# Performance work log

Hardware: AMD Instinct MI355X
Metric: run time of the kernel (lower is better)

## Reference

```python
import jax, jax.numpy as jnp
import numpy as np

B, S, D, H = 2, 2048, 2048, 16
HD = D // H
FF = 4 * D
EPS = 1e-5
SCALE = 1.0 / np.sqrt(D)  # source uses 1/sqrt(d_out), not 1/sqrt(head_dim)


def _gelu_tanh(x):
    c = np.sqrt(2.0 / np.pi).astype(np.float32)
    return 0.5 * x * (1.0 + jnp.tanh(c * (x + 0.044715 * x * x * x)))


def _layernorm(x, scale, shift):
    mean = jnp.mean(x, axis=-1, keepdims=True)
    var = jnp.mean(jnp.square(x - mean), axis=-1, keepdims=True)  # correction=0
    return (x - mean) * jax.lax.rsqrt(var + EPS) * scale + shift


def setup_inputs() -> dict:
    key = jax.random.key(0)
    ks = jax.random.split(key, 10)
    init = lambda k, shape, fan_in: (jax.random.normal(k, shape, jnp.float32) / np.sqrt(fan_in))
    return {
        "x": jax.random.normal(ks[0], (B, S, D), jnp.float32),
        "wq": init(ks[1], (D, D), D),
        "wk": init(ks[2], (D, D), D),
        "wv": init(ks[3], (D, D), D),
        "wo": init(ks[4], (D, D), D),
        "bo": jnp.zeros((D,), jnp.float32),
        "g1": jnp.ones((D,), jnp.float32),
        "s1": jnp.zeros((D,), jnp.float32),
        "g2": jnp.ones((D,), jnp.float32),
        "s2": jnp.zeros((D,), jnp.float32),
        "w1": init(ks[5], (D, FF), D),
        "b1": jnp.zeros((FF,), jnp.float32),
        "w2": init(ks[6], (FF, D), FF),
        "b2": jnp.zeros((D,), jnp.float32),
    }


def _block(x, wq, wk, wv, wo, bo, g1, s1, g2, s2, w1, b1, w2, b2):
    # pre-LN attention
    h = _layernorm(x, g1, s1)
    q = (h @ wq).reshape(B, S, H, HD).transpose(0, 2, 1, 3)  # [B,H,S,HD]
    k = (h @ wk).reshape(B, S, H, HD).transpose(0, 2, 1, 3)
    v = (h @ wv).reshape(B, S, H, HD).transpose(0, 2, 1, 3)
    scores = jnp.einsum('bhqd,bhkd->bhqk', q, k) * SCALE
    causal = jnp.tril(jnp.ones((S, S), dtype=bool))  # mask strictly-upper
    scores = jnp.where(causal, scores, -jnp.inf)
    attn = jax.nn.softmax(scores, axis=-1)
    ctx = jnp.einsum('bhqk,bhkd->bhqd', attn, v)
    ctx = ctx.transpose(0, 2, 1, 3).reshape(B, S, D)
    x = x + ctx @ wo + bo
    # pre-LN FFN
    h = _layernorm(x, g2, s2)
    h = _gelu_tanh(h @ w1 + b1) @ w2 + b2
    return x + h


def reference(x, wq, wk, wv, wo, bo, g1, s1, g2, s2, w1, b1, w2, b2):
    return _block(x, wq, wk, wv, wo, bo, g1, s1, g2, s2, w1, b1, w2, b2)
```

## Files before the change

kernel.cpp:

```cpp
#include <hip/hip_runtime.h>
#include <hip/hip_bf16.h>
#include <cstdint>

constexpr float SCALE_QK = 0.02209708691207961f;

using short8 = __attribute__((ext_vector_type(8))) short;
using f32x4  = __attribute__((ext_vector_type(4))) float;
using ushort4v = __attribute__((ext_vector_type(4))) ushort;

#define MFMA16(a,b,c) __builtin_amdgcn_mfma_f32_16x16x32_bf16((a),(b),(c),0,0,0)

__device__ __forceinline__ ushort f2bf(float f){
  uint32_t u = __builtin_bit_cast(uint32_t, f);
  u += 0x7fffu + ((u >> 16) & 1u);
  return (ushort)(u >> 16);
}

__device__ __forceinline__ void gload_lds16(const void* g, void* l){
  __builtin_amdgcn_global_load_lds(
      (const __attribute__((address_space(1))) void*)g,
      (__attribute__((address_space(3))) void*)l, 16, 0, 0);
}

__global__ __launch_bounds__(256) void ln_kernel(
    const float* __restrict__ x, const float* __restrict__ g,
    const float* __restrict__ sh, ushort* __restrict__ out){
  const int row = blockIdx.x, t = threadIdx.x;
  const float* xr = x + (size_t)row*2048 + t*8;
  float v[8];
  *(float4*)&v[0] = *(const float4*)(xr);
  *(float4*)&v[4] = *(const float4*)(xr + 4);
  float s = 0.f, sq = 0.f;
#pragma unroll
  for (int i = 0; i < 8; ++i){ s += v[i]; sq += v[i]*v[i]; }
#pragma unroll
  for (int d = 1; d < 64; d <<= 1){ s += __shfl_xor(s, d, 64); sq += __shfl_xor(sq, d, 64); }
  __shared__ float red[8];
  const int w = t >> 6, lane = t & 63;
  if (lane == 0){ red[w] = s; red[4 + w] = sq; }
  __syncthreads();
  s  = red[0] + red[1] + red[2] + red[3];
  sq = red[4] + red[5] + red[6] + red[7];
  const float mean = s * (1.f/2048.f);
  const float inv  = rsqrtf(sq * (1.f/2048.f) - mean*mean + 1e-5f);
  union { ushort u[8]; uint4 v4; } o;
#pragma unroll
  for (int i = 0; i < 8; ++i){
    int j = t*8 + i;
    o.u[i] = f2bf((v[i] - mean) * inv * g[j] + sh[j]);
  }
  *(uint4*)(out + (size_t)row*2048 + t*8) = o.v4;
}

__global__ __launch_bounds__(256) void wconv_t(
    const float* __restrict__ in, ushort* __restrict__ out, int K, int N){
  __shared__ ushort tile[32][34];
  const int tx = threadIdx.x & 31, ty = threadIdx.x >> 5;
  const int n0 = blockIdx.x * 32, k0 = blockIdx.y * 32;
#pragma unroll
  for (int r = 0; r < 4; ++r){
    int kk = ty + r*8;
    tile[kk][tx] = f2bf(in[(size_t)(k0 + kk)*N + n0 + tx]);
  }
  __syncthreads();
#pragma unroll
  for (int r = 0; r < 4; ++r){
    int nn = ty + r*8;
    out[(size_t)(n0 + nn)*K + k0 + tx] = tile[tx][nn];
  }
}

template<int EPI>
__global__ __launch_bounds__(256) void gemm_bt(
    const ushort* __restrict__ A, const ushort* __restrict__ Bt,
    int N, int K, void* __restrict__ outp,
    const float* __restrict__ resid, const float* __restrict__ bias){
  __shared__ ushort lds[2][128*64];
  const int tid = threadIdx.x, lane = tid & 63, wid = tid >> 6;
  const int wr = wid >> 1, wc = wid & 1;
  const int l15 = lane & 15, l4 = lane >> 4;

  const int bid = blockIdx.x;
  const int xcd = bid & 7, j = bid >> 3;
  const int mb = xcd*4 + (j & 3);
  const int nb = j >> 2;
  const int m0 = mb * 128, n0 = nb * 128;

  f32x4 acc[4][4];
#pragma unroll
  for (int mi = 0; mi < 4; ++mi)
#pragma unroll
    for (int ni = 0; ni < 4; ++ni) acc[mi][ni] = (f32x4){0.f,0.f,0.f,0.f};

  const ushort* Abase = A  + (size_t)m0*K;
  const ushort* Bbase = Bt + (size_t)n0*K;

  const int NTk = K >> 6;
  for (int kt = 0; kt < NTk; ++kt){
    if (kt) __syncthreads();
#pragma unroll
    for (int i = 0; i < 4; ++i){
      const int chunk = (i*4 + wid)*64 + lane;
      const int row = chunk >> 3;
      const int c8  = (chunk & 7) ^ (row & 7);
      const size_t goff = (size_t)row*K + (size_t)kt*64 + c8*8;
      gload_lds16(Abase + goff, (ushort*)&lds[0][0] + (size_t)(i*4 + wid)*512);
      gload_lds16(Bbase + goff, (ushort*)&lds[1][0] + (size_t)(i*4 + wid)*512);
    }
    __syncthreads();

#pragma unroll
    for (int kk = 0; kk < 2; ++kk){
      short8 af[4], bf[4];
      const int kb = kk*4 + l4;
#pragma unroll
      for (int i = 0; i < 4; ++i){
        const int rA = wr*64 + i*16 + l15;
        af[i] = *(const short8*)&lds[0][rA*64 + ((kb ^ (rA & 7))*8)];
        const int rB = wc*64 + i*16 + l15;
        bf[i] = *(const short8*)&lds[1][rB*64 + ((kb ^ (rB & 7))*8)];
      }
#pragma unroll
      for (int mi = 0; mi < 4; ++mi)
#pragma unroll
        for (int ni = 0; ni < 4; ++ni)
          acc[mi][ni] = MFMA16(af[mi], bf[ni], acc[mi][ni]);
    }
  }

#pragma unroll
  for (int mi = 0; mi < 4; ++mi){
#pragma unroll
    for (int ni = 0; ni < 4; ++ni){
      const int rloc = wr*64 + mi*16 + l4*4;
      const int col  = n0 + wc*64 + ni*16 + l15;
      if constexpr (EPI == 0){
        const int which = col >> 11, rest = col & 2047;
        const int h = rest >> 7, d = rest & 127;
        const int mrow = m0 + rloc;
        const int b = mrow >> 11, s = mrow & 2047;
        if (which == 2){
          ushort4v o;
#pragma unroll
          for (int j2 = 0; j2 < 4; ++j2) o[j2] = f2bf(acc[mi][ni][j2]);
          *(ushort4v*)&((ushort*)outp)[(size_t)2*8388608 +
              (size_t)(b*16 + h)*262144 + (size_t)d*2048 + s] = o;
        } else {
#pragma unroll
          for (int j2 = 0; j2 < 4; ++j2)
            ((ushort*)outp)[(size_t)which*8388608 +
                (((size_t)(b*16 + h)*2048 + (s + j2)) << 7) + d] = f2bf(acc[mi][ni][j2]);
        }
      } else {
#pragma unroll
        for (int j2 = 0; j2 < 4; ++j2){
          const int m = m0 + rloc + j2;
          float v = acc[mi][ni][j2];
          if constexpr (EPI == 1){
            ((float*)outp)[(size_t)m*N + col] = resid[(size_t)m*N + col] + bias[col] + v;
          } else {
            const float xx = v + bias[col];
            const float z  = 0.7978845608f*(xx + 0.044715f*xx*xx*xx);
            const float t  = __expf(-2.f*fabsf(z));
            const float th = (1.f - t)/(1.f + t);
            const float gl = 0.5f*xx*(1.f + copysignf(th, xx));
            ((ushort*)outp)[(size_t)m*N + col] = f2bf(gl);
          }
        }
      }
    }
  }
}

__global__ __launch_bounds__(256, 2) void attn_kernel(
    const ushort* __restrict__ q, const ushort* __restrict__ k,
    const ushort* __restrict__ vt, ushort* __restrict__ ctx){
  __shared__ ushort k_lds[2][64*128];
  __shared__ ushort v_lds[2][128*64];
  __shared__ ushort p_lds[4][32*64];
  const int tid = threadIdx.x, lane = tid & 63, w = tid >> 6;
  const int l15 = lane & 15, l4 = lane >> 4;
  const int id = blockIdx.x;
  const int bh = id & 31;
  const int r  = id >> 5;
  const int qt = (r < 8) ? (15 - r) : (r - 8);
  const int bb = bh >> 4, hh = bh & 15;
  const ushort* kbase = k  + (size_t)bh * 262144;
  const ushort* vbase = vt + (size_t)bh * 262144;

  short8 qf[2][4];
#pragma unroll
  for (int mi = 0; mi < 2; ++mi){
    const int s = qt*128 + w*32 + mi*16 + l15;
    const ushort* qr = q + ((size_t)bh*2048 + s)*128 + l4*8;
#pragma unroll
    for (int kk = 0; kk < 4; ++kk) qf[mi][kk] = *(const short8*)(qr + kk*32);
  }

  f32x4 cacc[2][8];
#pragma unroll
  for (int mi = 0; mi < 2; ++mi)
#pragma unroll
    for (int dt = 0; dt < 8; ++dt) cacc[mi][dt] = (f32x4){0.f,0.f,0.f,0.f};
  float mrun[2][4], lrun[2][4];
#pragma unroll
  for (int mi = 0; mi < 2; ++mi)
#pragma unroll
    for (int j = 0; j < 4; ++j){ mrun[mi][j] = -1e30f; lrun[mi][j] = 0.f; }

  auto stage = [&](int buf, int t){
    const ushort* ksrc = kbase + (size_t)t*8192;
#pragma unroll
    for (int i = 0; i < 4; ++i){
      const int base = i*256 + w*64;
      const int chunk = base + lane;
      const int kr = chunk >> 4;
      const int c8 = (chunk & 15) ^ (kr & 7);
      gload_lds16(ksrc + (size_t)kr*128 + c8*8, &k_lds[buf][(size_t)base*8]);
    }
#pragma unroll
    for (int i = 0; i < 4; ++i){
      const int base = i*256 + w*64;
      const int chunk = base + lane;
      const int vr = chunk >> 3;
      const int c8 = (chunk & 7) ^ (vr & 7);
      gload_lds16(vbase + (size_t)vr*2048 + t*64 + c8*8, &v_lds[buf][(size_t)base*8]);
    }
  };

  const int nt = 2*qt + 2;
  stage(0, 0);
  __syncthreads();
  int cur = 0;
  for (int t = 0; t < nt; ++t){
    if (t + 1 < nt) stage(cur ^ 1, t + 1);

    f32x4 sa[2][4];
#pragma unroll
    for (int mi = 0; mi < 2; ++mi)
#pragma unroll
      for (int ct = 0; ct < 4; ++ct) sa[mi][ct] = (f32x4){0.f,0.f,0.f,0.f};
    __builtin_amdgcn_s_setprio(1);
#pragma unroll
    for (int kk = 0; kk < 4; ++kk){
#pragma unroll
      for (int ct = 0; ct < 4; ++ct){
        const int kr = ct*16 + l15;
        short8 kf = *(const short8*)&k_lds[cur][kr*128 + (((kk*4 + l4) ^ (kr & 7))*8)];
        sa[0][ct] = MFMA16(qf[0][kk], kf, sa[0][ct]);
        sa[1][ct] = MFMA16(qf[1][kk], kf, sa[1][ct]);
      }
    }
    __builtin_amdgcn_s_setprio(0);

    const bool diag = (t >= 2*qt);
#pragma unroll
    for (int mi = 0; mi < 2; ++mi){
#pragma unroll
      for (int j = 0; j < 4; ++j){
        const int qa = qt*128 + w*32 + mi*16 + l4*4 + j;
        float mnew = mrun[mi][j];
#pragma unroll
        for (int ct = 0; ct < 4; ++ct){
          float sc = sa[mi][ct][j] * SCALE_QK;
          if (diag){
            const int ka = t*64 + ct*16 + l15;
            sc = (ka > qa) ? -1e30f : sc;
          }
          sa[mi][ct][j] = sc;
          mnew = fmaxf(mnew, sc);
        }
#pragma unroll
        for (int d = 1; d < 16; d <<= 1) mnew = fmaxf(mnew, __shfl_xor(mnew, d, 16));
        const float corr = __expf(mrun[mi][j] - mnew);
        mrun[mi][j] = mnew; lrun[mi][j] *= corr;
        float psum = 0.f;
#pragma unroll
        for (int ct = 0; ct < 4; ++ct){
          const float p = __expf(sa[mi][ct][j] - mnew);
          sa[mi][ct][j] = p; psum += p;
        }
        lrun[mi][j] += psum;
#pragma unroll
        for (int dt = 0; dt < 8; ++dt) cacc[mi][dt][j] *= corr;
      }
    }

#pragma unroll
    for (int mi = 0; mi < 2; ++mi)
#pragma unroll
      for (int ct = 0; ct < 4; ++ct)
#pragma unroll
        for (int j = 0; j < 4; ++j){
          const int row = mi*16 + l4*4 + j, col = ct*16 + l15;
          p_lds[w][row*64 + ((col >> 3) ^ (row & 7))*8 + (col & 7)] = f2bf(sa[mi][ct][j]);
        }

    __builtin_amdgcn_s_setprio(1);
#pragma unroll
    for (int kk2 = 0; kk2 < 2; ++kk2){
      const int kb = kk2*4 + l4;
      short8 pa0 = *(const short8*)&p_lds[w][l15*64 + ((kb ^ (l15 & 7))*8)];
      short8 pa1 = *(const short8*)&p_lds[w][(16 + l15)*64 + ((kb ^ (l15 & 7))*8)];
#pragma unroll
      for (int dt = 0; dt < 8; ++dt){
        const int vr = dt*16 + l15;
        short8 vf = *(const short8*)&v_lds[cur][vr*64 + ((kb ^ (vr & 7))*8)];
        cacc[0][dt] = MFMA16(pa0, vf, cacc[0][dt]);
        cacc[1][dt] = MFMA16(pa1, vf, cacc[1][dt]);
      }
    }
    __builtin_amdgcn_s_setprio(0);

    if (t + 1 < nt){ __syncthreads(); cur ^= 1; }
  }

#pragma unroll
  for (int mi = 0; mi < 2; ++mi){
    float inv[4];
#pragma unroll
    for (int j = 0; j < 4; ++j){
      float lt = lrun[mi][j];
#pragma unroll
      for (int d = 1; d < 16; d <<= 1) lt += __shfl_xor(lt, d, 16);
      inv[j] = 1.f / lt;
    }
#pragma unroll
    for (int dt = 0; dt < 8; ++dt)
#pragma unroll
      for (int j = 0; j < 4; ++j){
        const int s = qt*128 + w*32 + mi*16 + l4*4 + j;
        const int d = dt*16 + l15;
        ctx[((size_t)(bb*2048 + s))*2048 + hh*128 + d] = f2bf(cacc[mi][dt][j] * inv[j]);
      }
  }
}

extern "C" void kernel_launch(void* const* d_in, const int* in_sizes, int n_in,
                              void* d_out, int out_size, void* d_ws, size_t ws_size,
                              hipStream_t stream) {
  const float* x  = (const float*)d_in[0];
  const float* wq = (const float*)d_in[1];
  const float* wk = (const float*)d_in[2];
  const float* wv = (const float*)d_in[3];
  const float* wo = (const float*)d_in[4];
  const float* bo = (const float*)d_in[5];
  const float* g1 = (const float*)d_in[6];
  const float* s1 = (const float*)d_in[7];
  const float* g2 = (const float*)d_in[8];
  const float* s2 = (const float*)d_in[9];
  const float* w1 = (const float*)d_in[10];
  const float* b1 = (const float*)d_in[11];
  const float* w2 = (const float*)d_in[12];
  const float* b2 = (const float*)d_in[13];
  float* out = (float*)d_out;
  char* ws = (char*)d_ws;

  ushort* wqkvT = (ushort*)(ws + 0);
  ushort* wkT = (ushort*)(ws + 8388608);
  ushort* wvT = (ushort*)(ws + 16777216);
  ushort* woT = (ushort*)(ws + 25165824);
  ushort* w1T = (ushort*)(ws + 33554432);
  ushort* w2T = (ushort*)(ws + 67108864);
  ushort* h1  = (ushort*)(ws + 100663296);
  ushort* qb  = (ushort*)(ws + 117440512);
  ushort* kb  = (ushort*)(ws + 134217728);
  ushort* vtb = (ushort*)(ws + 150994944);
  ushort* ctxb= (ushort*)(ws + 184549376);
  float*  x2  = (float*)(ws + 201326592);
  ushort* h2  = (ushort*)(ws + 234881024);
  ushort* ffb = (ushort*)(ws + 117440512);

  wconv_t<<<dim3(64, 64), 256, 0, stream>>>(wq, wqkvT, 2048, 2048);
  wconv_t<<<dim3(64, 64), 256, 0, stream>>>(wk, wkT, 2048, 2048);
  wconv_t<<<dim3(64, 64), 256, 0, stream>>>(wv, wvT, 2048, 2048);
  wconv_t<<<dim3(64, 64), 256, 0, stream>>>(wo, woT, 2048, 2048);
  wconv_t<<<dim3(256, 64), 256, 0, stream>>>(w1, w1T, 2048, 8192);
  wconv_t<<<dim3(64, 256), 256, 0, stream>>>(w2, w2T, 8192, 2048);

  ln_kernel<<<4096, 256, 0, stream>>>(x, g1, s1, h1);

  gemm_bt<0><<<32*48, 256, 0, stream>>>(h1, wqkvT, 6144, 2048, qb, nullptr, nullptr);

  attn_kernel<<<512, 256, 0, stream>>>(qb, kb, vtb, ctxb);

  gemm_bt<1><<<32*16, 256, 0, stream>>>(ctxb, woT, 2048, 2048, x2, x, bo);

  ln_kernel<<<4096, 256, 0, stream>>>(x2, g2, s2, h2);

  gemm_bt<2><<<32*64, 256, 0, stream>>>(h2, w1T, 8192, 2048, ffb, nullptr, b1);
  gemm_bt<1><<<32*16, 256, 0, stream>>>(ffb, w2T, 2048, 8192, out, x2, b2);

  (void)in_sizes; (void)n_in; (void)out_size; (void)ws_size;
}
```

Baseline: 694.9 us.

## Add 256x256-tile 8-wave ping-pong GEMM for QKV and FFN-up projections

Introduces a new GEMM kernel with 512 threads and 256x256 output tiles split into four 128x128 quadrants. It double-buffers A and B halves in LDS and interleaves global-to-LDS staging with MFMA phases, using explicit vmcnt waits, barriers and s_setprio. The QKV and FFN-up GEMMs now use it, which raises data reuse per block and overlaps loads with compute. The cost is a large LDS footprint (128KB) and register pressure at 2 blocks per CU, plus many barriers per k-step; the old gemm_bt loses its now-unused epilogue branches.

```diff
diff --git a/kernel.cpp b/kernel.cpp
--- a/kernel.cpp
+++ b/kernel.cpp
@@ -21,6 +21,11 @@
       (const __attribute__((address_space(1))) void*)g,
       (__attribute__((address_space(3))) void*)l, 16, 0, 0);
 }
+
+#define VMCNT(n) asm volatile("s_waitcnt vmcnt(" #n ")" ::: "memory")
+#define BAR() do{ __builtin_amdgcn_s_barrier(); \
+  asm volatile("" ::: "memory"); \
+  __builtin_amdgcn_sched_barrier(0); }while(0)
 
 __global__ __launch_bounds__(256) void ln_kernel(
     const float* __restrict__ x, const float* __restrict__ g,
@@ -70,6 +75,148 @@
   }
 }
 
+#define MM(qd) do{ __builtin_amdgcn_s_setprio(1); \
+  _Pragma("unroll") for (int mi = 0; mi < 4; ++mi) \
+  _Pragma("unroll") for (int ni = 0; ni < 2; ++ni) \
+  _Pragma("unroll") for (int kk = 0; kk < 2; ++kk) \
+    acc[qd][mi][ni] = MFMA16(af[mi][kk], bf[ni][kk], acc[qd][mi][ni]); \
+  __builtin_amdgcn_s_setprio(0); }while(0)
+
+template<int EPI>
+__global__ __launch_bounds__(512, 2) void gemm8p(
+    const ushort* __restrict__ A, const ushort* __restrict__ Bt,
+    int N, int K, void* __restrict__ outp, const float* __restrict__ bias){
+  __shared__ ushort Al[2][2][128*64];
+  __shared__ ushort Bl[2][2][128*64];
+  const int tid = threadIdx.x, lane = tid & 63, wid = tid >> 6;
+  const int l15 = lane & 15, l4 = lane >> 4;
+  const int wrr = wid >> 2, wcc = wid & 3;
+
+  const int bid = blockIdx.x;
+  const int xcd = bid & 7, jj = bid >> 3;
+  const int m0 = (xcd*2 + (jj & 1)) * 256;
+  const int n0 = (jj >> 1) * 256;
+
+  const ushort* Abase = A  + (size_t)m0*K;
+  const ushort* Bbase = Bt + (size_t)n0*K;
+
+  f32x4 acc[4][4][2];
+#pragma unroll
+  for (int q = 0; q < 4; ++q)
+#pragma unroll
+    for (int mi = 0; mi < 4; ++mi)
+#pragma unroll
+      for (int ni = 0; ni < 2; ++ni) acc[q][mi][ni] = (f32x4){0.f,0.f,0.f,0.f};
+
+  auto stageA = [&](int buf, int h, int kt){
+#pragma unroll
+    for (int l = 0; l < 2; ++l){
+      const int c = l*512 + tid, r = c >> 3, s = (c & 7) ^ ((c >> 3) & 7);
+      gload_lds16(Abase + (size_t)(h*128 + r)*K + (size_t)kt*64 + s*8,
+                  &Al[buf][h][c*8]);
+    }
+  };
+  auto stageB = [&](int buf, int h, int kt){
+#pragma unroll
+    for (int l = 0; l < 2; ++l){
+      const int c = l*512 + tid, r = c >> 3, s = (c & 7) ^ ((c >> 3) & 7);
+      gload_lds16(Bbase + (size_t)(h*128 + r)*K + (size_t)kt*64 + s*8,
+                  &Bl[buf][h][c*8]);
+    }
+  };
+
+  short8 af[4][2], bf[2][2];
+  auto readA = [&](int buf, int h){
+#pragma unroll
+    for (int mi = 0; mi < 4; ++mi){
+      const int r = wrr*64 + mi*16 + l15;
+#pragma unroll
+      for (int kk = 0; kk < 2; ++kk)
+        af[mi][kk] = *(const short8*)&Al[buf][h][r*64 + (((kk*4 + l4) ^ (r & 7))*8)];
+    }
+  };
+  auto readB = [&](int buf, int h){
+#pragma unroll
+    for (int ni = 0; ni < 2; ++ni){
+      const int r = wcc*32 + ni*16 + l15;
+#pragma unroll
+      for (int kk = 0; kk < 2; ++kk)
+        bf[ni][kk] = *(const short8*)&Bl[buf][h][r*64 + (((kk*4 + l4) ^ (r & 7))*8)];
+    }
+  };
+
+  const int NT = K >> 6;
+  stageA(0,0,0); stageB(0,0,0); stageB(0,1,0); stageA(0,1,0);
+  VMCNT(4); BAR();
+
+  for (int kt = 0; kt < NT - 1; ++kt){
+    const int cur = kt & 1, nxt = cur ^ 1;
+    readA(cur,0); readB(cur,0);
+    stageA(nxt,0,kt+1);
+    VMCNT(4); BAR();
+    MM(0); BAR();
+    readB(cur,1);
+    stageB(nxt,0,kt+1);
+    VMCNT(4); BAR();
+    MM(1); BAR();
+    readA(cur,1);
+    stageB(nxt,1,kt+1);
+    BAR();
+    MM(2); BAR();
+    readB(cur,0);
+    stageA(nxt,1,kt+1);
+    VMCNT(4); BAR();
+    MM(3); BAR();
+  }
+  {
+    const int cur = (NT - 1) & 1;
+    readA(cur,0); readB(cur,0); VMCNT(2); BAR(); MM(0); BAR();
+    readB(cur,1);               VMCNT(0); BAR(); MM(1); BAR();
+    readA(cur,1);                         BAR(); MM(2); BAR();
+    readB(cur,0);                         BAR(); MM(3); BAR();
+  }
+
+#pragma unroll
+  for (int qd = 0; qd < 4; ++qd){
+    const int qr = qd >> 1, qc = qr ^ (qd & 1);
+#pragma unroll
+    for (int mi = 0; mi < 4; ++mi){
+#pragma unroll
+      for (int ni = 0; ni < 2; ++ni){
+        const int mrow = m0 + qr*128 + wrr*64 + mi*16 + l4*4;
+        const int col  = n0 + qc*128 + wcc*32 + ni*16 + l15;
+        if constexpr (EPI == 0){
+          const int which = col >> 11, rest = col & 2047;
+          const int h = rest >> 7, d = rest & 127;
+          const int b = mrow >> 11, s = mrow & 2047;
+          if (which == 2){
+            ushort4v o;
+#pragma unroll
+            for (int j2 = 0; j2 < 4; ++j2) o[j2] = f2bf(acc[qd][mi][ni][j2]);
+            *(ushort4v*)&((ushort*)outp)[(size_t)2*8388608 +
+                (size_t)(b*16 + h)*262144 + (size_t)d*2048 + s] = o;
+          } else {
+#pragma unroll
+            for (int j2 = 0; j2 < 4; ++j2)
+              ((ushort*)outp)[(size_t)which*8388608 +
+                  (((size_t)(b*16 + h)*2048 + (s + j2)) << 7) + d] = f2bf(acc[qd][mi][ni][j2]);
+          }
+        } else {
+#pragma unroll
+          for (int j2 = 0; j2 < 4; ++j2){
+            const float xx = acc[qd][mi][ni][j2] + bias[col];
+            const float z  = 0.7978845608f*(xx + 0.044715f*xx*xx*xx);
+            const float t  = __expf(-2.f*fabsf(z));
+            const float th = (1.f - t)/(1.f + t);
+            const float gl = 0.5f*xx*(1.f + copysignf(th, xx));
+            ((ushort*)outp)[(size_t)(mrow + j2)*N + col] = f2bf(gl);
+          }
+        }
+      }
+    }
+  }
+}
+
 template<int EPI>
 __global__ __launch_bounds__(256) void gemm_bt(
     const ushort* __restrict__ A, const ushort* __restrict__ Bt,
@@ -134,38 +281,14 @@
     for (int ni = 0; ni < 4; ++ni){
       const int rloc = wr*64 + mi*16 + l4*4;
       const int col  = n0 + wc*64 + ni*16 + l15;
-      if constexpr (EPI == 0){
-        const int which = col >> 11, rest = col & 2047;
-        const int h = rest >> 7, d = rest & 127;
-        const int mrow = m0 + rloc;
-        const int b = mrow >> 11, s = mrow & 2047;
-        if (which == 2){
-          ushort4v o;
-#pragma unroll
-          for (int j2 = 0; j2 < 4; ++j2) o[j2] = f2bf(acc[mi][ni][j2]);
-          *(ushort4v*)&((ushort*)outp)[(size_t)2*8388608 +
-              (size_t)(b*16 + h)*262144 + (size_t)d*2048 + s] = o;
+#pragma unroll
+      for (int j2 = 0; j2 < 4; ++j2){
+        const int m = m0 + rloc + j2;
+        float v = acc[mi][ni][j2];
+        if constexpr (EPI == 1){
+          ((float*)outp)[(size_t)m*N + col] = resid[(size_t)m*N + col] + bias[col] + v;
         } else {
-#pragma unroll
-          for (int j2 = 0; j2 < 4; ++j2)
-            ((ushort*)outp)[(size_t)which*8388608 +
-                (((size_t)(b*16 + h)*2048 + (s + j2)) << 7) + d] = f2bf(acc[mi][ni][j2]);
-        }
-      } else {
-#pragma unroll
-        for (int j2 = 0; j2 < 4; ++j2){
-          const int m = m0 + rloc + j2;
-          float v = acc[mi][ni][j2];
-          if constexpr (EPI == 1){
-            ((float*)outp)[(size_t)m*N + col] = resid[(size_t)m*N + col] + bias[col] + v;
-          } else {
-            const float xx = v + bias[col];
-            const float z  = 0.7978845608f*(xx + 0.044715f*xx*xx*xx);
-            const float t  = __expf(-2.f*fabsf(z));
-            const float th = (1.f - t)/(1.f + t);
-            const float gl = 0.5f*xx*(1.f + copysignf(th, xx));
-            ((ushort*)outp)[(size_t)m*N + col] = f2bf(gl);
-          }
+          ((ushort*)outp)[(size_t)m*N + col] = f2bf(v);
         }
       }
     }
@@ -380,7 +503,7 @@
 
   ln_kernel<<<4096, 256, 0, stream>>>(x, g1, s1, h1);
 
-  gemm_bt<0><<<32*48, 256, 0, stream>>>(h1, wqkvT, 6144, 2048, qb, nullptr, nullptr);
+  gemm8p<0><<<384, 512, 0, stream>>>(h1, wqkvT, 6144, 2048, qb, nullptr);
 
   attn_kernel<<<512, 256, 0, stream>>>(qb, kb, vtb, ctxb);
 
@@ -388,7 +511,7 @@
 
   ln_kernel<<<4096, 256, 0, stream>>>(x2, g2, s2, h2);
 
-  gemm_bt<2><<<32*64, 256, 0, stream>>>(h2, w1T, 8192, 2048, ffb, nullptr, b1);
+  gemm8p<2><<<512, 512, 0, stream>>>(h2, w1T, 8192, 2048, ffb, b1);
   gemm_bt<1><<<32*16, 256, 0, stream>>>(ffb, w2T, 2048, 8192, out, x2, b2);
 
   (void)in_sizes; (void)n_in; (void)out_size; (void)ws_size;
```

Result: slower. 754.4 us (+8.6%).

## Stage QKV epilogue through LDS for coalesced stores and skip fully masked attention tiles

Applied to the files above, without the earlier changes.

The QKV GEMM epilogue now writes each output tile into LDS first, transposed for V, and then issues coalesced 16-byte global stores in place of scattered 2-byte or 8-byte writes. The softmax scale is folded into Q at the GEMM epilogue, which removes a multiply per score in attention. In the attention loop, warps whose query rows lie entirely before the last key tile skip that fully masked tile, and warps that need no mask on the first diagonal tile skip the mask compare. This adds extra barriers and reuses LDS in the GEMM epilogue, and it creates some warp divergence within the attention block.

```diff
diff --git a/kernel.cpp b/kernel.cpp
--- a/kernel.cpp
+++ b/kernel.cpp
@@ -128,30 +128,60 @@
     }
   }
 
-#pragma unroll
-  for (int mi = 0; mi < 4; ++mi){
-#pragma unroll
-    for (int ni = 0; ni < 4; ++ni){
-      const int rloc = wr*64 + mi*16 + l4*4;
-      const int col  = n0 + wc*64 + ni*16 + l15;
-      if constexpr (EPI == 0){
-        const int which = col >> 11, rest = col & 2047;
-        const int h = rest >> 7, d = rest & 127;
-        const int mrow = m0 + rloc;
-        const int b = mrow >> 11, s = mrow & 2047;
-        if (which == 2){
+  if constexpr (EPI == 0){
+    __syncthreads();
+    ushort* tile = (ushort*)&lds[0][0];
+    const int which = n0 >> 11;
+    const int hh = (n0 & 2047) >> 7;
+    const int bb = m0 >> 11, srow0 = m0 & 2047;
+    if (which != 2){
+      const float qs = (which == 0) ? SCALE_QK : 1.0f;
+#pragma unroll
+      for (int mi = 0; mi < 4; ++mi)
+#pragma unroll
+        for (int ni = 0; ni < 4; ++ni){
+          const int rl = wr*64 + mi*16 + l4*4;
+          const int cl = wc*64 + ni*16 + l15;
+#pragma unroll
+          for (int j2 = 0; j2 < 4; ++j2)
+            tile[(rl + j2)*128 + cl] = f2bf(acc[mi][ni][j2] * qs);
+        }
+      __syncthreads();
+      ushort* dst = (ushort*)outp + (size_t)which*8388608 +
+                    ((size_t)(bb*16 + hh)*2048 + srow0)*128;
+#pragma unroll
+      for (int i = 0; i < 8; ++i){
+        const int c = i*256 + tid, row = c >> 4, d8 = (c & 15)*8;
+        *(uint4*)(dst + (size_t)row*128 + d8) = *(const uint4*)&tile[row*128 + d8];
+      }
+    } else {
+#pragma unroll
+      for (int mi = 0; mi < 4; ++mi)
+#pragma unroll
+        for (int ni = 0; ni < 4; ++ni){
+          const int rl = wr*64 + mi*16 + l4*4;
+          const int cl = wc*64 + ni*16 + l15;
           ushort4v o;
 #pragma unroll
           for (int j2 = 0; j2 < 4; ++j2) o[j2] = f2bf(acc[mi][ni][j2]);
-          *(ushort4v*)&((ushort*)outp)[(size_t)2*8388608 +
-              (size_t)(b*16 + h)*262144 + (size_t)d*2048 + s] = o;
-        } else {
-#pragma unroll
-          for (int j2 = 0; j2 < 4; ++j2)
-            ((ushort*)outp)[(size_t)which*8388608 +
-                (((size_t)(b*16 + h)*2048 + (s + j2)) << 7) + d] = f2bf(acc[mi][ni][j2]);
-        }
-      } else {
+          *(ushort4v*)&tile[cl*128 + rl] = o;
+        }
+      __syncthreads();
+      ushort* dst = (ushort*)outp + (size_t)2*8388608 +
+                    (size_t)(bb*16 + hh)*262144 + srow0;
+#pragma unroll
+      for (int i = 0; i < 8; ++i){
+        const int c = i*256 + tid, drow = c >> 4, s8 = (c & 15)*8;
+        *(uint4*)(dst + (size_t)drow*2048 + s8) = *(const uint4*)&tile[drow*128 + s8];
+      }
+    }
+  } else {
+#pragma unroll
+    for (int mi = 0; mi < 4; ++mi){
+#pragma unroll
+      for (int ni = 0; ni < 4; ++ni){
+        const int rloc = wr*64 + mi*16 + l4*4;
+        const int col  = n0 + wc*64 + ni*16 + l15;
 #pragma unroll
         for (int j2 = 0; j2 < 4; ++j2){
           const int m = m0 + rloc + j2;
@@ -235,82 +265,85 @@
   for (int t = 0; t < nt; ++t){
     if (t + 1 < nt) stage(cur ^ 1, t + 1);
 
-    f32x4 sa[2][4];
-#pragma unroll
-    for (int mi = 0; mi < 2; ++mi)
-#pragma unroll
-      for (int ct = 0; ct < 4; ++ct) sa[mi][ct] = (f32x4){0.f,0.f,0.f,0.f};
-    __builtin_amdgcn_s_setprio(1);
-#pragma unroll
-    for (int kk = 0; kk < 4; ++kk){
-#pragma unroll
-      for (int ct = 0; ct < 4; ++ct){
-        const int kr = ct*16 + l15;
-        short8 kf = *(const short8*)&k_lds[cur][kr*128 + (((kk*4 + l4) ^ (kr & 7))*8)];
-        sa[0][ct] = MFMA16(qf[0][kk], kf, sa[0][ct]);
-        sa[1][ct] = MFMA16(qf[1][kk], kf, sa[1][ct]);
-      }
-    }
-    __builtin_amdgcn_s_setprio(0);
-
-    const bool diag = (t >= 2*qt);
-#pragma unroll
-    for (int mi = 0; mi < 2; ++mi){
-#pragma unroll
-      for (int j = 0; j < 4; ++j){
-        const int qa = qt*128 + w*32 + mi*16 + l4*4 + j;
-        float mnew = mrun[mi][j];
+    const bool skip = (t == 2*qt + 1) && (w < 2);
+    if (!skip){
+      f32x4 sa[2][4];
+#pragma unroll
+      for (int mi = 0; mi < 2; ++mi)
+#pragma unroll
+        for (int ct = 0; ct < 4; ++ct) sa[mi][ct] = (f32x4){0.f,0.f,0.f,0.f};
+      __builtin_amdgcn_s_setprio(1);
+#pragma unroll
+      for (int kk = 0; kk < 4; ++kk){
 #pragma unroll
         for (int ct = 0; ct < 4; ++ct){
-          float sc = sa[mi][ct][j] * SCALE_QK;
-          if (diag){
-            const int ka = t*64 + ct*16 + l15;
-            sc = (ka > qa) ? -1e30f : sc;
+          const int kr = ct*16 + l15;
+          short8 kf = *(const short8*)&k_lds[cur][kr*128 + (((kk*4 + l4) ^ (kr & 7))*8)];
+          sa[0][ct] = MFMA16(qf[0][kk], kf, sa[0][ct]);
+          sa[1][ct] = MFMA16(qf[1][kk], kf, sa[1][ct]);
+        }
+      }
+      __builtin_amdgcn_s_setprio(0);
+
+      const bool anymask = (t >= 2*qt) && !((t == 2*qt) && (w >= 2));
+#pragma unroll
+      for (int mi = 0; mi < 2; ++mi){
+#pragma unroll
+        for (int j = 0; j < 4; ++j){
+          const int qa = qt*128 + w*32 + mi*16 + l4*4 + j;
+          float mnew = mrun[mi][j];
+#pragma unroll
+          for (int ct = 0; ct < 4; ++ct){
+            float sc = sa[mi][ct][j];
+            if (anymask){
+              const int ka = t*64 + ct*16 + l15;
+              sc = (ka > qa) ? -1e30f : sc;
+            }
+            sa[mi][ct][j] = sc;
+            mnew = fmaxf(mnew, sc);
           }
-          sa[mi][ct][j] = sc;
-          mnew = fmaxf(mnew, sc);
-        }
-#pragma unroll
-        for (int d = 1; d < 16; d <<= 1) mnew = fmaxf(mnew, __shfl_xor(mnew, d, 16));
-        const float corr = __expf(mrun[mi][j] - mnew);
-        mrun[mi][j] = mnew; lrun[mi][j] *= corr;
-        float psum = 0.f;
-#pragma unroll
-        for (int ct = 0; ct < 4; ++ct){
-          const float p = __expf(sa[mi][ct][j] - mnew);
-          sa[mi][ct][j] = p; psum += p;
-        }
-        lrun[mi][j] += psum;
-#pragma unroll
-        for (int dt = 0; dt < 8; ++dt) cacc[mi][dt][j] *= corr;
-      }
-    }
-
-#pragma unroll
-    for (int mi = 0; mi < 2; ++mi)
-#pragma unroll
-      for (int ct = 0; ct < 4; ++ct)
-#pragma unroll
-        for (int j = 0; j < 4; ++j){
-          const int row = mi*16 + l4*4 + j, col = ct*16 + l15;
-          p_lds[w][row*64 + ((col >> 3) ^ (row & 7))*8 + (col & 7)] = f2bf(sa[mi][ct][j]);
-        }
-
-    __builtin_amdgcn_s_setprio(1);
-#pragma unroll
-    for (int kk2 = 0; kk2 < 2; ++kk2){
-      const int kb = kk2*4 + l4;
-      short8 pa0 = *(const short8*)&p_lds[w][l15*64 + ((kb ^ (l15 & 7))*8)];
-      short8 pa1 = *(const short8*)&p_lds[w][(16 + l15)*64 + ((kb ^ (l15 & 7))*8)];
-#pragma unroll
-      for (int dt = 0; dt < 8; ++dt){
-        const int vr = dt*16 + l15;
-        short8 vf = *(const short8*)&v_lds[cur][vr*64 + ((kb ^ (vr & 7))*8)];
-        cacc[0][dt] = MFMA16(pa0, vf, cacc[0][dt]);
-        cacc[1][dt] = MFMA16(pa1, vf, cacc[1][dt]);
-      }
-    }
-    __builtin_amdgcn_s_setprio(0);
+#pragma unroll
+          for (int d = 1; d < 16; d <<= 1) mnew = fmaxf(mnew, __shfl_xor(mnew, d, 16));
+          const float corr = __expf(mrun[mi][j] - mnew);
+          mrun[mi][j] = mnew; lrun[mi][j] *= corr;
+          float psum = 0.f;
+#pragma unroll
+          for (int ct = 0; ct < 4; ++ct){
+            const float p = __expf(sa[mi][ct][j] - mnew);
+            sa[mi][ct][j] = p; psum += p;
+          }
+          lrun[mi][j] += psum;
+#pragma unroll
+          for (int dt = 0; dt < 8; ++dt) cacc[mi][dt][j] *= corr;
+        }
+      }
+
+#pragma unroll
+      for (int mi = 0; mi < 2; ++mi)
+#pragma unroll
+        for (int ct = 0; ct < 4; ++ct)
+#pragma unroll
+          for (int j = 0; j < 4; ++j){
+            const int row = mi*16 + l4*4 + j, col = ct*16 + l15;
+            p_lds[w][row*64 + ((col >> 3) ^ (row & 7))*8 + (col & 7)] = f2bf(sa[mi][ct][j]);
+          }
+
+      __builtin_amdgcn_s_setprio(1);
+#pragma unroll
+      for (int kk2 = 0; kk2 < 2; ++kk2){
+        const int kb = kk2*4 + l4;
+        short8 pa0 = *(const short8*)&p_lds[w][l15*64 + ((kb ^ (l15 & 7))*8)];
+        short8 pa1 = *(const short8*)&p_lds[w][(16 + l15)*64 + ((kb ^ (l15 & 7))*8)];
+#pragma unroll
+        for (int dt = 0; dt < 8; ++dt){
+          const int vr = dt*16 + l15;
+          short8 vf = *(const short8*)&v_lds[cur][vr*64 + ((kb ^ (vr & 7))*8)];
+          cacc[0][dt] = MFMA16(pa0, vf, cacc[0][dt]);
+          cacc[1][dt] = MFMA16(pa1, vf, cacc[1][dt]);
+        }
+      }
+      __builtin_amdgcn_s_setprio(0);
+    }
 
     if (t + 1 < nt){ __syncthreads(); cur ^= 1; }
   }
```

Result: no change. 688.7 us (-0.9%).
